# Performance work log

Hardware: AMD Instinct MI355X
Metric: run time of the kernel (lower is better)

The kernel has to match this reference:

```python
import jax, jax.numpy as jnp
import numpy as np

N_OD = 4000  # number of OD pairs (rows of incidence matrix M)


def setup_inputs() -> dict:
    key = jax.random.key(0)
    k1, k2, k3, k4, k5, k6 = jax.random.split(key, 6)
    X = jax.random.normal(k1, (64, 24, 500, 5), dtype=jnp.float32)          # (days, hours, links, features)
    theta = jax.random.normal(k2, (5,), dtype=jnp.float32)                   # utility coefficients
    theta_links = 0.1 * jax.random.normal(k3, (500,), dtype=jnp.float32)     # per-link utility offsets
    q_sqrt = jax.random.uniform(k4, (4000,), dtype=jnp.float32)              # sqrt of OD demand q
    D = jax.random.uniform(k5, (500, 20000), dtype=jnp.float32)              # link-path incidence (n_links, n_paths)
    seg_ids = jnp.sort(jax.random.randint(k6, (20000,), 0, N_OD)).astype(jnp.int32)  # OD group of each path (sorted, as in M row-major nnz order)
    return {"X": X, "theta": theta, "theta_links": theta_links,
            "q_sqrt": q_sqrt, "D": D, "seg_ids": seg_ids}


def reference(X, theta, theta_links, q_sqrt, D, seg_ids):
    # project_theta: all feature signs '-' -> clip to (-inf, 0]
    theta_c = jnp.minimum(theta, jnp.zeros((), theta.dtype))
    # link_utilities: einsum('ijkl,l->ijk', X, theta) + theta_links
    v_links = jnp.einsum('dhlf,f->dhl', X, theta_c) + theta_links            # (days, hours, links)
    d, h, L = v_links.shape
    P = D.shape[1]
    B = d * h
    # path_utilities: einsum('ijk,kl->ijl', V, D)
    vp = jnp.einsum('dhl,lp->dhp', v_links, D).reshape(B, P)                 # (B, n_paths)
    # path_probabilities_sparse with normalization=True:
    # grouped softmax over paths sharing an OD pair (segments = seg_ids),
    # group-max is wrapped in stop_gradient as in the TF code.
    neg_inf = jnp.finfo(vp.dtype).min
    gmax = jnp.full((B, N_OD), neg_inf, vp.dtype).at[:, seg_ids].max(vp)     # sparse.reduce_max over axis=3
    e = jnp.exp(vp - jax.lax.stop_gradient(gmax[:, seg_ids]))
    denom = jnp.zeros((B, N_OD), vp.dtype).at[:, seg_ids].add(e)             # sparse.reduce_sum over axis=3
    pf = e / denom[:, seg_ids]                                               # path probabilities
    # path_flows: f_p = q_{od(p)} * pf_p  (== einsum('ij,i,klj->klj', M, q, pf))
    q = q_sqrt * q_sqrt
    f = pf * q[seg_ids]                                                      # (B, n_paths)
    # link_flows: einsum('ijk,lk->ijl', f, D)
    out = jnp.einsum('bp,lp->bl', f, D).reshape(d, h, L)                     # (days, hours, links)
    return out
```

## Files before the change

kernel.cpp:

```cpp
#include <hip/hip_runtime.h>
#include <hip/hip_bf16.h>
#include <stdint.h>

#define M_B   1536
#define N_L   500
#define N_LP  512
#define N_P   20000
#define N_PP  20096
#define N_G   4000
#define SPLITK 16
#define KCHUNK2 1280
#define NQW   32
#define GQW   (N_G / NQW)
#define NCH   4
#define SVC   1024
#define NT1   (N_PP / 128)
#define MT1   (M_B / 128)
#define NB1   (NT1 * MT1)

#define OFF_A1   ((size_t)0)
#define OFF_D1   ((size_t)1572864)
#define OFF_DT   ((size_t)22151168)
#define OFF_VP   ((size_t)42729472)
#define OFF_PART OFF_VP
#define OFF_F    ((size_t)166199296)
#define OFF_BND  ((size_t)227934208)

typedef __bf16 bf16x8 __attribute__((ext_vector_type(8)));
typedef __bf16 bf16x4 __attribute__((ext_vector_type(4)));
typedef float  f32x4  __attribute__((ext_vector_type(4)));
typedef int    i32x4  __attribute__((ext_vector_type(4)));

__device__ __forceinline__ void gload16(const void* g, void* l) {
  __builtin_amdgcn_global_load_lds(
      (const __attribute__((address_space(1))) void*)g,
      (__attribute__((address_space(3))) void*)l, 16, 0, 0);
}

__global__ __launch_bounds__(256) void prep_a1(const float* __restrict__ X,
                                               const float* __restrict__ theta,
                                               const float* __restrict__ theta_links,
                                               __bf16* __restrict__ A1) {
  int idx = blockIdx.x * 256 + threadIdx.x;
  if (idx >= M_B * N_LP) return;
  int b = idx >> 9, l = idx & (N_LP - 1);
  float v = 0.f;
  if (l < N_L) {
    const float* x = X + ((size_t)b * N_L + l) * 5;
#pragma unroll
    for (int f = 0; f < 5; ++f) v += x[f] * fminf(theta[f], 0.f);
    v += theta_links[l];
  }
  A1[idx] = (__bf16)v;
}

__global__ __launch_bounds__(256) void prep_d(const float* __restrict__ D,
                                              __bf16* __restrict__ D1,
                                              __bf16* __restrict__ Dt) {
  __shared__ float t[32][33];
  int pb = blockIdx.x * 32;
  int lb = blockIdx.y * 32;
  for (int i = threadIdx.y; i < 32; i += 8) {
    int l = lb + i, p = pb + threadIdx.x;
    float v = (l < N_L && p < N_P) ? D[(size_t)l * N_P + p] : 0.f;
    t[i][threadIdx.x] = v;
    D1[(size_t)l * N_PP + p] = (__bf16)v;
  }
  __syncthreads();
  for (int i = threadIdx.y; i < 32; i += 8) {
    int p = pb + i, l = lb + threadIdx.x;
    Dt[(size_t)p * N_LP + l] = (__bf16)t[threadIdx.x][i];
  }
}

__global__ __launch_bounds__(256) void seg_bounds(const int* __restrict__ seg,
                                                  int* __restrict__ bounds) {
  int g = blockIdx.x * 256 + threadIdx.x;
  if (g > N_G) return;
  int lo = 0, hi = N_P;
  while (lo < hi) { int mid = (lo + hi) >> 1; if (seg[mid] < g) lo = mid + 1; else hi = mid; }
  bounds[g] = lo;
}

template <int MODE, int OBF>
__global__ __launch_bounds__(256) void gemm_bt(const __bf16* __restrict__ A,
                                               const __bf16* __restrict__ Bt,
                                               void* __restrict__ C,
                                               int lda, int ldb, int ldc,
                                               int K, int kchunk, size_t zstride) {
  int bx, by, bz;
  if (MODE == 1) {
    int x = blockIdx.x & 7, k = blockIdx.x >> 3;
    int start = (x < 4) ? 236 * x : 944 + 235 * (x - 4);
    int L = start + k;
    bx = L / MT1;  by = L - bx * MT1;  bz = 0;
  } else {
    int bid = blockIdx.x; bz = bid & 15; bx = (bid >> 4) & 3; by = bid >> 6;
  }
  __shared__ __bf16 lsA[128 * 32];
  __shared__ __bf16 lsB[128 * 32];
  const int tid = threadIdx.x;
  const int lane = tid & 63;
  const int wv = tid >> 6;
  const int wr = wv >> 1, wc = wv & 1;
  const int m0 = by * 128;
  const int n0 = bx * 128;
  const int kb = bz * kchunk;
  const int klen = min(kchunk, K - kb);

  const int srow = wv * 16 + (lane >> 2);
  const int scol = (lane & 3) * 8;
  const __bf16* gA = A + (size_t)(m0 + srow) * lda + kb + scol;
  const __bf16* gB = Bt + (size_t)(n0 + srow) * ldb + kb + scol;
  __bf16* lA0 = &lsA[(wv * 16) * 32];
  __bf16* lA1 = &lsA[(64 + wv * 16) * 32];
  __bf16* lB0 = &lsB[(wv * 16) * 32];
  __bf16* lB1 = &lsB[(64 + wv * 16) * 32];

  f32x4 acc[4][4] = {};
  const int fra = (wr * 64 + (lane & 15)) * 32 + 8 * (lane >> 4);
  const int frb = (wc * 64 + (lane & 15)) * 32 + 8 * (lane >> 4);

  for (int kk = 0; kk < klen; kk += 32) {
    gload16(gA + kk, lA0);
    gload16(gA + (size_t)64 * lda + kk, lA1);
    gload16(gB + kk, lB0);
    gload16(gB + (size_t)64 * ldb + kk, lB1);
    __syncthreads();
    bf16x8 av[4], bv[4];
#pragma unroll
    for (int r = 0; r < 4; ++r) av[r] = *(const bf16x8*)&lsA[fra + r * 16 * 32];
#pragma unroll
    for (int c = 0; c < 4; ++c) bv[c] = *(const bf16x8*)&lsB[frb + c * 16 * 32];
#pragma unroll
    for (int r = 0; r < 4; ++r)
#pragma unroll
      for (int c = 0; c < 4; ++c)
        acc[r][c] = __builtin_amdgcn_mfma_f32_16x16x32_bf16(av[r], bv[c], acc[r][c], 0, 0, 0);
    __syncthreads();
  }

  const int erow = m0 + wr * 64 + (lane >> 4) * 4;
  const int ecol = n0 + wc * 64 + (lane & 15);
#pragma unroll
  for (int r = 0; r < 4; ++r)
#pragma unroll
    for (int c = 0; c < 4; ++c) {
      if (OBF) {
        __bf16* p = (__bf16*)C + (size_t)(erow + r * 16) * ldc + (ecol + c * 16);
#pragma unroll
        for (int j = 0; j < 4; ++j) p[(size_t)j * ldc] = (__bf16)acc[r][c][j];
      } else {
        float* p = (float*)C + (size_t)bz * zstride +
                   (size_t)(erow + r * 16) * ldc + (ecol + c * 16);
#pragma unroll
        for (int j = 0; j < 4; ++j) p[(size_t)j * ldc] = acc[r][c][j];
      }
    }
}

__global__ __launch_bounds__(64) void seg_softmax(const __bf16* __restrict__ vp,
                                                  const int* __restrict__ bounds,
                                                  const int* __restrict__ seg,
                                                  const float* __restrict__ q_sqrt,
                                                  __bf16* __restrict__ f) {
  __shared__ float sv[SVC];
  __shared__ float ssc[GQW];
  const int tid = threadIdx.x;
  const int b = blockIdx.x;
  const int g0 = blockIdx.y * GQW;

  const int s0 = bounds[g0];
  const int e0 = (blockIdx.y == NQW - 1) ? N_P : bounds[g0 + GQW];
  const int s0a = s0 & ~3;
  const int e0a = (e0 + 3) & ~3;
  const __bf16* row = vp + (size_t)b * N_PP;

  for (int i = tid; i * 4 < e0a - s0a; i += 64) {
    bf16x4 v4 = *(const bf16x4*)&row[s0a + i * 4];
    f32x4 v;
#pragma unroll
    for (int j = 0; j < 4; ++j) v[j] = (float)v4[j];
    *(f32x4*)&sv[i * 4] = v;
  }
  __syncthreads();

#pragma unroll
  for (int round = 0; round < 2; ++round) {
    int g = g0 + round * 64 + tid;
    if (g < g0 + GQW) {
      int s = bounds[g], e = bounds[g + 1];
      float m = -3.4e38f;
      for (int p = s; p < e; ++p) m = fmaxf(m, sv[p - s0a]);
      float den = 0.f;
      for (int p = s; p < e; ++p) {
        float t = __expf(sv[p - s0a] - m);
        den += t;
        sv[p - s0a] = t;
      }
      float qs = q_sqrt[g];
      ssc[g - g0] = (s < e) ? qs * qs / den : 0.f;
    }
  }
  __syncthreads();

  __bf16* frow = f + (size_t)b * N_PP;
#pragma unroll
  for (int c = 0; c < NCH; ++c) {
    int p = s0a + (c * 64 + tid) * 4;
    if (p >= e0a) continue;
    f32x4 e4 = *(const f32x4*)&sv[p - s0a];
    i32x4 sgv = *(const i32x4*)&seg[p];
    bf16x4 o;
    bool ok[4];
#pragma unroll
    for (int j = 0; j < 4; ++j) {
      int gi = sgv[j] - g0;
      ok[j] = (unsigned)gi < (unsigned)GQW;
      int idx = ok[j] ? gi : 0;
      o[j] = (__bf16)(e4[j] * ssc[idx]);
    }
    if (ok[0] && ok[3]) {
      *(bf16x4*)&frow[p] = o;
    } else {
#pragma unroll
      for (int j = 0; j < 4; ++j)
        if (ok[j]) frow[p + j] = o[j];
    }
  }
  if (blockIdx.y == NQW - 1)
    for (int p = N_P + tid; p < N_PP; p += 64) frow[p] = (__bf16)0.f;
}

__global__ __launch_bounds__(256) void reduce_out(const float* __restrict__ part,
                                                  float* __restrict__ out) {
  int idx = blockIdx.x * 256 + threadIdx.x;
  if (idx >= M_B * N_L) return;
  int b = idx / N_L, l = idx - b * N_L;
  float s = 0.f;
#pragma unroll
  for (int z = 0; z < SPLITK; ++z)
    s += part[(size_t)z * M_B * N_LP + (size_t)b * N_LP + l];
  out[idx] = s;
}

extern "C" void kernel_launch(void* const* d_in, const int* in_sizes, int n_in,
                              void* d_out, int out_size, void* d_ws, size_t ws_size,
                              hipStream_t stream) {
  const float* X           = (const float*)d_in[0];
  const float* theta       = (const float*)d_in[1];
  const float* theta_links = (const float*)d_in[2];
  const float* q_sqrt      = (const float*)d_in[3];
  const float* D           = (const float*)d_in[4];
  const int*   seg         = (const int*)d_in[5];
  float* out = (float*)d_out;

  char* ws = (char*)d_ws;
  __bf16* A1   = (__bf16*)(ws + OFF_A1);
  __bf16* D1   = (__bf16*)(ws + OFF_D1);
  __bf16* Dt   = (__bf16*)(ws + OFF_DT);
  __bf16* vp   = (__bf16*)(ws + OFF_VP);
  float*  part = (float*)(ws + OFF_PART);
  __bf16* fbuf = (__bf16*)(ws + OFF_F);
  int*    bnd  = (int*)(ws + OFF_BND);

  prep_a1<<<(M_B * N_LP) / 256, 256, 0, stream>>>(X, theta, theta_links, A1);
  prep_d<<<dim3(N_PP / 32, N_LP / 32), dim3(32, 8), 0, stream>>>(D, D1, Dt);
  seg_bounds<<<16, 256, 0, stream>>>(seg, bnd);

  gemm_bt<1, 1><<<dim3(NB1, 1, 1), 256, 0, stream>>>(
      A1, Dt, vp, N_LP, N_LP, N_PP, N_LP, N_LP, (size_t)0);

  seg_softmax<<<dim3(M_B, NQW), 64, 0, stream>>>(vp, bnd, seg, q_sqrt, fbuf);

  gemm_bt<2, 0><<<dim3((N_LP / 128) * (M_B / 128) * SPLITK, 1, 1), 256, 0, stream>>>(
      fbuf, D1, part, N_PP, N_PP, N_LP, N_PP, KCHUNK2, (size_t)(M_B * N_LP));

  reduce_out<<<(M_B * N_L + 255) / 256, 256, 0, stream>>>(part, out);
}
```

Measured before the change: 184.2 us.

## Double-buffer LDS tiles in bf16 GEMM to overlap loads with MFMA

Splits the shared-memory A/B tiles into two buffers so the next K-slice is fetched with direct global-to-LDS loads while MFMAs run on the current slice. This cuts the loop to one barrier per iteration and hides global load latency behind compute. It doubles LDS use per block, which may lower occupancy, and correctness relies on the async loads being properly waited on before the barrier.

```diff
diff --git a/kernel.cpp b/kernel.cpp
--- a/kernel.cpp
+++ b/kernel.cpp
@@ -97,8 +97,8 @@
   } else {
     int bid = blockIdx.x; bz = bid & 15; bx = (bid >> 4) & 3; by = bid >> 6;
   }
-  __shared__ __bf16 lsA[128 * 32];
-  __shared__ __bf16 lsB[128 * 32];
+  __shared__ __bf16 lsA[2][128 * 32];
+  __shared__ __bf16 lsB[2][128 * 32];
   const int tid = threadIdx.x;
   const int lane = tid & 63;
   const int wv = tid >> 6;
@@ -110,35 +110,50 @@
 
   const int srow = wv * 16 + (lane >> 2);
   const int scol = (lane & 3) * 8;
+  const int sb = (wv * 16) * 32;
   const __bf16* gA = A + (size_t)(m0 + srow) * lda + kb + scol;
   const __bf16* gB = Bt + (size_t)(n0 + srow) * ldb + kb + scol;
-  __bf16* lA0 = &lsA[(wv * 16) * 32];
-  __bf16* lA1 = &lsA[(64 + wv * 16) * 32];
-  __bf16* lB0 = &lsB[(wv * 16) * 32];
-  __bf16* lB1 = &lsB[(64 + wv * 16) * 32];
 
   f32x4 acc[4][4] = {};
   const int fra = (wr * 64 + (lane & 15)) * 32 + 8 * (lane >> 4);
   const int frb = (wc * 64 + (lane & 15)) * 32 + 8 * (lane >> 4);
 
-  for (int kk = 0; kk < klen; kk += 32) {
-    gload16(gA + kk, lA0);
-    gload16(gA + (size_t)64 * lda + kk, lA1);
-    gload16(gB + kk, lB0);
-    gload16(gB + (size_t)64 * ldb + kk, lB1);
+#define STAGE(buf, kk)                                                        \
+  {                                                                           \
+    gload16(gA + (kk), &lsA[buf][sb]);                                        \
+    gload16(gA + (size_t)64 * lda + (kk), &lsA[buf][64 * 32 + sb]);           \
+    gload16(gB + (kk), &lsB[buf][sb]);                                        \
+    gload16(gB + (size_t)64 * ldb + (kk), &lsB[buf][64 * 32 + sb]);           \
+  }
+#define COMPUTE(buf)                                                          \
+  {                                                                           \
+    bf16x8 av[4], bv[4];                                                      \
+    _Pragma("unroll")                                                         \
+    for (int r = 0; r < 4; ++r)                                               \
+      av[r] = *(const bf16x8*)&lsA[buf][fra + r * 16 * 32];                   \
+    _Pragma("unroll")                                                         \
+    for (int c = 0; c < 4; ++c)                                               \
+      bv[c] = *(const bf16x8*)&lsB[buf][frb + c * 16 * 32];                   \
+    _Pragma("unroll")                                                         \
+    for (int r = 0; r < 4; ++r)                                               \
+      _Pragma("unroll")                                                       \
+      for (int c = 0; c < 4; ++c)                                             \
+        acc[r][c] = __builtin_amdgcn_mfma_f32_16x16x32_bf16(av[r], bv[c],     \
+                                                            acc[r][c], 0, 0, 0); \
+  }
+
+  STAGE(0, 0);
+  __syncthreads();
+  int cur = 0;
+  for (int kk = 32; kk < klen; kk += 32) {
+    STAGE(cur ^ 1, kk);
+    COMPUTE(cur);
     __syncthreads();
-    bf16x8 av[4], bv[4];
-#pragma unroll
-    for (int r = 0; r < 4; ++r) av[r] = *(const bf16x8*)&lsA[fra + r * 16 * 32];
-#pragma unroll
-    for (int c = 0; c < 4; ++c) bv[c] = *(const bf16x8*)&lsB[frb + c * 16 * 32];
-#pragma unroll
-    for (int r = 0; r < 4; ++r)
-#pragma unroll
-      for (int c = 0; c < 4; ++c)
-        acc[r][c] = __builtin_amdgcn_mfma_f32_16x16x32_bf16(av[r], bv[c], acc[r][c], 0, 0, 0);
-    __syncthreads();
-  }
+    cur ^= 1;
+  }
+  COMPUTE(cur);
+#undef STAGE
+#undef COMPUTE
 
   const int erow = m0 + wr * 64 + (lane >> 4) * 4;
   const int ecol = n0 + wc * 64 + (lane & 15);
```

After: 177.6 us. 3.6% less time.
